# Kernel optimization log

Hardware: AMD Instinct MI355X
Metric: run time of the kernel (lower is better)

Reference implementation:

```python
import jax, jax.numpy as jnp
import numpy as np

N_NODES = 50000
N_EDGES = 400000
IN_DIM = 256
HID = 64
N_CLASSES = 121


def setup_inputs() -> dict:
    key = jax.random.key(0)
    ks = jax.random.split(key, 16)
    inp = {
        "features": jax.random.normal(ks[0], (N_NODES, IN_DIM), jnp.float32),
        "src": jax.random.randint(ks[1], (N_EDGES,), 0, N_NODES, jnp.int32),
        "dst": jax.random.randint(ks[2], (N_EDGES,), 0, N_NODES, jnp.int32),
        # layer 0: 4 heads, in_dim -> hid, no residual
        "W0": jax.random.normal(ks[3], (4, HID, IN_DIM), jnp.float32) * 0.05,
        "al0": jax.random.normal(ks[4], (4, HID), jnp.float32) * 0.05,
        "ar0": jax.random.normal(ks[5], (4, HID), jnp.float32) * 0.05,
        # layer 1: 4 heads, 4*hid -> hid, residual via fc
        "W1": jax.random.normal(ks[6], (4, HID, 4 * HID), jnp.float32) * 0.05,
        "al1": jax.random.normal(ks[7], (4, HID), jnp.float32) * 0.05,
        "ar1": jax.random.normal(ks[8], (4, HID), jnp.float32) * 0.05,
        "R1": jax.random.normal(ks[9], (4, HID, 4 * HID), jnp.float32) * 0.05,
        # final: 6 heads, 4*hid -> classes, residual via fc, averaged
        "Wf": jax.random.normal(ks[10], (6, N_CLASSES, 4 * HID), jnp.float32) * 0.05,
        "alf": jax.random.normal(ks[11], (6, N_CLASSES), jnp.float32) * 0.05,
        "arf": jax.random.normal(ks[12], (6, N_CLASSES), jnp.float32) * 0.05,
        "Rf": jax.random.normal(ks[13], (6, N_CLASSES, 4 * HID), jnp.float32) * 0.05,
    }
    return inp


def _gat_layer(x, src, dst, W, al, ar, R, n_nodes):
    """Multi-head GAT layer. x:[N,D], W:[H,K,D], al/ar:[H,K], R:[H,K,D] or None.
    Returns [N,H,K] = activation(residual + edge-softmax-weighted neighbor sum)."""
    ft = jnp.einsum('nd,hkd->nhk', x, W)              # [N,H,K]
    a1 = jnp.einsum('nhk,hk->nh', ft, al)             # [N,H] attn_l(ft)
    a2 = jnp.einsum('nhk,hk->nh', ft, ar)             # [N,H] attn_r(ft)
    # per-edge score: leaky_relu(a1[dst] + a2[src]) (DGL mailbox softmax over in-edges)
    s = jax.nn.leaky_relu(a1[dst] + a2[src], negative_slope=0.01)   # [E,H]
    smax = jax.ops.segment_max(s, dst, num_segments=n_nodes)        # [N,H]
    smax = jnp.where(jnp.isfinite(smax), smax, 0.0)
    ex = jnp.exp(s - smax[dst])                                     # [E,H]
    denom = jax.ops.segment_sum(ex, dst, num_segments=n_nodes)      # [N,H]
    msg = ex[:, :, None] * ft[src]                                  # [E,H,K]
    accum = jax.ops.segment_sum(msg, dst, num_segments=n_nodes)     # [N,H,K]
    accum = accum / jnp.where(denom > 0, denom, 1.0)[:, :, None]
    if R is not None:
        accum = accum + jnp.einsum('nd,hkd->nhk', x, R)
    return jax.nn.elu(accum)


def reference(features, src, dst, W0, al0, ar0, W1, al1, ar1, R1, Wf, alf, arf, Rf):
    n = features.shape[0]
    h0 = _gat_layer(features, src, dst, W0, al0, ar0, None, n)  # [N,4,64]
    h0 = h0.reshape(n, -1)                                      # concat heads -> [N,256]
    h1 = _gat_layer(h0, src, dst, W1, al1, ar1, R1, n)          # [N,4,64]
    h1 = h1.reshape(n, -1)                                      # [N,256]
    hf = _gat_layer(h1, src, dst, Wf, alf, arf, Rf, n)          # [N,6,121]
    return hf.mean(axis=1)                                      # average final heads -> [N,121]
```

## Files before the change

### kernel.cpp

```cpp
#include <hip/hip_runtime.h>
#include <math.h>

#define NN 50000
#define NE 400000
#define NB ((NN + 255) / 256)

typedef __attribute__((ext_vector_type(8))) short bf16x8;
typedef __attribute__((ext_vector_type(4))) float f32x4;
#define AS1 __attribute__((address_space(1)))
#define AS3 __attribute__((address_space(3)))

__device__ __forceinline__ float lrelu(float x){ return x > 0.0f ? x : 0.01f*x; }
__device__ __forceinline__ float eluf(float x){ return x > 0.0f ? x : __expf(x)-1.0f; }
__device__ __forceinline__ float bf2f(unsigned short u){
  union{unsigned i; float f;} v; v.i = ((unsigned)u)<<16; return v.f;
}
__device__ __forceinline__ unsigned short f2bf(float x){
  union{float f; unsigned i;} v; v.f = x;
  unsigned r = v.i + 0x7FFFu + ((v.i>>16)&1u);
  return (unsigned short)(r>>16);
}
__device__ __forceinline__ unsigned pack2(float a, float b){
  return (unsigned)f2bf(a) | ((unsigned)f2bf(b)<<16);
}
__device__ __forceinline__ float lo16(unsigned u){ return bf2f((unsigned short)(u & 0xffffu)); }
__device__ __forceinline__ float hi16(unsigned u){ return bf2f((unsigned short)(u >> 16)); }

__global__ void k_diag(float* out, float val){ out[0] = val; }

__global__ void k_cvt(const float* __restrict__ in, unsigned short* __restrict__ o, int n){
  int i = (blockIdx.x*256 + threadIdx.x)*4;
  if(i + 3 < n){
    float4 v = *(const float4*)(in + i);
    uint2 p; p.x = pack2(v.x, v.y); p.y = pack2(v.z, v.w);
    *(uint2*)(o + i) = p;
  } else {
    for(int k = i; k < n; k++) o[k] = f2bf(in[k]);
  }
}

__global__ void k_cvt3(const float* __restrict__ s0, const float* __restrict__ s1,
    const float* __restrict__ s2, unsigned short* __restrict__ d0,
    unsigned short* __restrict__ d1, unsigned short* __restrict__ d2, int n){
  const float* in = (blockIdx.y == 0) ? s0 : (blockIdx.y == 1) ? s1 : s2;
  unsigned short* o = (blockIdx.y == 0) ? d0 : (blockIdx.y == 1) ? d1 : d2;
  int i = (blockIdx.x*256 + threadIdx.x)*4;
  if(i + 3 < n){
    float4 v = *(const float4*)(in + i);
    uint2 p; p.x = pack2(v.x, v.y); p.y = pack2(v.z, v.w);
    *(uint2*)(o + i) = p;
  } else {
    for(int k = i; k < n; k++) o[k] = f2bf(in[k]);
  }
}

__global__ void k_cvt2(const float* __restrict__ s0, const float* __restrict__ s1,
    unsigned short* __restrict__ d0, unsigned short* __restrict__ d1, int n){
  const float* in = (blockIdx.y == 0) ? s0 : s1;
  unsigned short* o = (blockIdx.y == 0) ? d0 : d1;
  int i = (blockIdx.x*256 + threadIdx.x)*4;
  if(i + 3 < n){
    float4 v = *(const float4*)(in + i);
    uint2 p; p.x = pack2(v.x, v.y); p.y = pack2(v.z, v.w);
    *(uint2*)(o + i) = p;
  } else {
    for(int k = i; k < n; k++) o[k] = f2bf(in[k]);
  }
}

__global__ void k_foldAll(const float* __restrict__ W0, const float* __restrict__ al0, const float* __restrict__ ar0,
    const float* __restrict__ W1, const float* __restrict__ al1, const float* __restrict__ ar1,
    const float* __restrict__ Wf, const float* __restrict__ alf, const float* __restrict__ arf,
    float* __restrict__ fl0, float* __restrict__ fr0, float* __restrict__ fl1, float* __restrict__ fr1,
    float* __restrict__ flF, float* __restrict__ frF){
  int b = blockIdx.x, d = threadIdx.x;
  const float *W, *al, *ar; float *fl, *fr; int K, h;
  if(b < 4){ W=W0; al=al0; ar=ar0; fl=fl0; fr=fr0; K=64; h=b; }
  else if(b < 8){ W=W1; al=al1; ar=ar1; fl=fl1; fr=fr1; K=64; h=b-4; }
  else { W=Wf; al=alf; ar=arf; fl=flF; fr=frF; K=121; h=b-8; }
  float sl = 0.f, sr = 0.f;
  const float* wb = W + ((size_t)h*K)*256 + d;
  for(int k = 0; k < K; k++){
    float w = wb[(size_t)k*256];
    sl += al[h*K + k]*w;
    sr += ar[h*K + k]*w;
  }
  fl[h*256 + d] = sl;
  fr[h*256 + d] = sr;
}

__global__ void k_count(const int* __restrict__ dst, int* __restrict__ cnt, int E){
  int e = blockIdx.x * 256 + threadIdx.x;
  if(e < E) atomicAdd(&cnt[dst[e]], 1);
}

__global__ void k_scanA(const int* __restrict__ cnt, int* __restrict__ row_ptr,
    int* __restrict__ bsum, int N){
  __shared__ int sh[256];
  int t = threadIdx.x;
  int i = blockIdx.x*256 + t;
  int v = (i < N) ? cnt[i] : 0;
  sh[t] = v;
  __syncthreads();
  for(int off = 1; off < 256; off <<= 1){
    int u = (t >= off) ? sh[t - off] : 0;
    __syncthreads();
    sh[t] += u;
    __syncthreads();
  }
  if(i < N) row_ptr[i] = sh[t] - v;
  if(t == 255) bsum[blockIdx.x] = sh[255];
}

__global__ void k_scanB(const int* __restrict__ bsum, int* __restrict__ boff, int nb){
  __shared__ int sh[256];
  int t = threadIdx.x;
  int v = (t < nb) ? bsum[t] : 0;
  sh[t] = v;
  __syncthreads();
  for(int off = 1; off < 256; off <<= 1){
    int u = (t >= off) ? sh[t - off] : 0;
    __syncthreads();
    sh[t] += u;
    __syncthreads();
  }
  if(t < nb) boff[t] = sh[t] - v;
  if(t == 255) boff[nb] = sh[255];
}

__global__ void k_scanC(int* __restrict__ row_ptr, const int* __restrict__ boff, int N, int nb){
  int i = blockIdx.x*256 + threadIdx.x;
  if(i < N) row_ptr[i] += boff[blockIdx.x];
  if(i == 0) row_ptr[N] = boff[nb];
}

__global__ void k_scatter(const int* __restrict__ src, const int* __restrict__ dst,
    const int* __restrict__ row_ptr, int* __restrict__ cur,
    int* __restrict__ col_src, int* __restrict__ col_dst, int E){
  int e = blockIdx.x * 256 + threadIdx.x;
  if(e < E){
    int d = dst[e];
    int pos = row_ptr[d] + atomicAdd(&cur[d], 1);
    col_src[pos] = src[e];
    col_dst[pos] = d;
  }
}

template<int S>
__global__ __launch_bounds__(256) void k_eexp(const int* __restrict__ col_src, const int* __restrict__ col_dst,
    const float* __restrict__ a1, const float* __restrict__ a2, float* __restrict__ ex){
  int p = blockIdx.x*256 + threadIdx.x;
  if(p >= NE) return;
  int s = col_src[p], d = col_dst[p];
  if(S == 4){
    float4 v1 = *(const float4*)(a1 + (size_t)d*4);
    float4 v2 = *(const float4*)(a2 + (size_t)s*4);
    float4 o;
    o.x = __expf(lrelu(v1.x + v2.x));
    o.y = __expf(lrelu(v1.y + v2.y));
    o.z = __expf(lrelu(v1.z + v2.z));
    o.w = __expf(lrelu(v1.w + v2.w));
    *(float4*)(ex + (size_t)p*4) = o;
  } else {
    float4 l1 = *(const float4*)(a1 + (size_t)d*8);
    float2 h1 = *(const float2*)(a1 + (size_t)d*8 + 4);
    float4 l2 = *(const float4*)(a2 + (size_t)s*8);
    float2 h2 = *(const float2*)(a2 + (size_t)s*8 + 4);
    float4 o;
    o.x = __expf(lrelu(l1.x + l2.x));
    o.y = __expf(lrelu(l1.y + l2.y));
    o.z = __expf(lrelu(l1.z + l2.z));
    o.w = __expf(lrelu(l1.w + l2.w));
    float2 o2;
    o2.x = __expf(lrelu(h1.x + h2.x));
    o2.y = __expf(lrelu(h1.y + h2.y));
    *(float4*)(ex + (size_t)p*8) = o;
    *(float2*)(ex + (size_t)p*8 + 4) = o2;
  }
}

__global__ __launch_bounds__(256) void k_gemm16(const unsigned short* __restrict__ X,
    const unsigned short* __restrict__ W, unsigned short* __restrict__ out,
    int N, int Kout, int ostride){
  __shared__ unsigned short sA[4096];
  __shared__ unsigned short sB[4096];
  int tid = threadIdx.x;
  int l = tid & 63, w = tid >> 6;
  int wm = w >> 1, wn = w & 1;
  int row0 = blockIdx.x*128, col0 = blockIdx.y*128;

  f32x4 acc[4][4];
  #pragma unroll
  for(int i=0;i<4;i++)
    #pragma unroll
    for(int j=0;j<4;j++) acc[i][j] = (f32x4){0.f,0.f,0.f,0.f};

  int grA0 = row0 + l;        if(grA0 >= N) grA0 = 0;
  int grA1 = row0 + 64 + l;   if(grA1 >= N) grA1 = 0;
  int gcB0 = col0 + l;        if(gcB0 >= Kout) gcB0 = 0;
  int gcB1 = col0 + 64 + l;   if(gcB1 >= Kout) gcB1 = 0;
  const unsigned short* pa0 = X + (size_t)grA0*256 + w*8;
  const unsigned short* pa1 = X + (size_t)grA1*256 + w*8;
  const unsigned short* pb0 = W + (size_t)gcB0*256 + w*8;
  const unsigned short* pb1 = W + (size_t)gcB1*256 + w*8;

  AS3 unsigned short* a3A = (AS3 unsigned short*)sA;
  AS3 unsigned short* a3B = (AS3 unsigned short*)sB;

  for(int kt = 0; kt < 256; kt += 32){
    __builtin_amdgcn_global_load_lds((const AS1 void*)(pa0 + kt), (AS3 void*)(a3A + w*1024),       16, 0, 0);
    __builtin_amdgcn_global_load_lds((const AS1 void*)(pa1 + kt), (AS3 void*)(a3A + w*1024 + 512), 16, 0, 0);
    __builtin_amdgcn_global_load_lds((const AS1 void*)(pb0 + kt), (AS3 void*)(a3B + w*1024),       16, 0, 0);
    __builtin_amdgcn_global_load_lds((const AS1 void*)(pb1 + kt), (AS3 void*)(a3B + w*1024 + 512), 16, 0, 0);
    __syncthreads();
    bf16x8 af[4], bfr[4];
    #pragma unroll
    for(int f=0; f<4; f++){
      af[f]  = *(const bf16x8*)(sA + (l>>4)*1024 + (wm*64 + f*16 + (l&15))*8);
      bfr[f] = *(const bf16x8*)(sB + (l>>4)*1024 + (wn*64 + f*16 + (l&15))*8);
    }
    #pragma unroll
    for(int i=0;i<4;i++)
      #pragma unroll
      for(int j=0;j<4;j++)
        acc[i][j] = __builtin_amdgcn_mfma_f32_16x16x32_bf16(af[i], bfr[j], acc[i][j], 0, 0, 0);
    __syncthreads();
  }

  #pragma unroll
  for(int i=0;i<4;i++){
    int rbase = row0 + wm*64 + i*16 + (l>>4)*4;
    #pragma unroll
    for(int j=0;j<4;j++){
      int c = col0 + wn*64 + j*16 + (l&15);
      if(c < Kout){
        #pragma unroll
        for(int q=0;q<4;q++){
          int r = rbase + q;
          if(r < N) out[(size_t)r*ostride + c] = f2bf(acc[i][j][q]);
        }
      }
    }
  }
}

__global__ __launch_bounds__(256) void k_gemmFh(const unsigned short* __restrict__ aggX,
    const unsigned short* __restrict__ xin, const unsigned short* __restrict__ wf,
    const unsigned short* __restrict__ rf, float* __restrict__ outp, int M){
  __shared__ unsigned short sA[8192];
  __shared__ unsigned short sB[8192];
  int tid = threadIdx.x;
  int l = tid & 63, w = tid >> 6;
  int wm = w >> 1, wn = w & 1;
  int h = blockIdx.y;
  int row0 = blockIdx.x*128;
  int rA0 = row0 + l;      if(rA0 >= M) rA0 = 0;
  int rA1 = row0 + 64 + l; if(rA1 >= M) rA1 = 0;
  int cB1 = 64 + l; if(cB1 > 120) cB1 = 120;

  AS3 unsigned short* a3A = (AS3 unsigned short*)sA;
  AS3 unsigned short* a3B = (AS3 unsigned short*)sB;

  f32x4 acc[4][4];
  #pragma unroll
  for(int i=0;i<4;i++)
    #pragma unroll
    for(int j=0;j<4;j++) acc[i][j] = (f32x4){0.f,0.f,0.f,0.f};

  #pragma unroll 1
  for(int ph = 0; ph < 2; ph++){
    const unsigned short* pa0 = (ph ? xin + (size_t)rA0*256 : aggX + (size_t)rA0*1536 + h*256) + w*8;
    const unsigned short* pa1 = (ph ? xin + (size_t)rA1*256 : aggX + (size_t)rA1*1536 + h*256) + w*8;
    const unsigned short* pbb = (ph ? rf : wf) + (size_t)h*121*256;
    const unsigned short* pb0 = pbb + (size_t)l*256 + w*8;
    const unsigned short* pb1 = pbb + (size_t)cB1*256 + w*8;
    #pragma unroll 1
    for(int kt = 0; kt < 256; kt += 64){
      #pragma unroll
      for(int jj = 0; jj < 2; jj++){
        int j = w + jj*4;
        int ko = kt + jj*32;
        __builtin_amdgcn_global_load_lds((const AS1 void*)(pa0 + ko), (AS3 void*)(a3A + j*1024),       16, 0, 0);
        __builtin_amdgcn_global_load_lds((const AS1 void*)(pa1 + ko), (AS3 void*)(a3A + j*1024 + 512), 16, 0, 0);
        __builtin_amdgcn_global_load_lds((const AS1 void*)(pb0 + ko), (AS3 void*)(a3B + j*1024),       16, 0, 0);
        __builtin_amdgcn_global_load_lds((const AS1 void*)(pb1 + ko), (AS3 void*)(a3B + j*1024 + 512), 16, 0, 0);
      }
      __syncthreads();
      #pragma unroll
      for(int ks = 0; ks < 2; ks++){
        bf16x8 af[4], bfr[4];
        #pragma unroll
        for(int f=0; f<4; f++){
          af[f]  = *(const bf16x8*)(sA + (ks*4 + (l>>4))*1024 + (wm*64 + f*16 + (l&15))*8);
          bfr[f] = *(const bf16x8*)(sB + (ks*4 + (l>>4))*1024 + (wn*64 + f*16 + (l&15))*8);
        }
        #pragma unroll
        for(int i=0;i<4;i++)
          #pragma unroll
          for(int j=0;j<4;j++)
            acc[i][j] = __builtin_amdgcn_mfma_f32_16x16x32_bf16(af[i], bfr[j], acc[i][j], 0, 0, 0);
      }
      __syncthreads();
    }
  }

  const float inv6 = 1.0f/6.0f;
  #pragma unroll
  for(int i=0;i<4;i++){
    int rbase = row0 + wm*64 + i*16 + (l>>4)*4;
    #pragma unroll
    for(int j=0;j<4;j++){
      int c = wn*64 + j*16 + (l&15);
      if(c < 121){
        #pragma unroll
        for(int q=0;q<4;q++){
          int r = rbase + q;
          if(r < M) atomicAdd(&outp[(size_t)r*121 + c], eluf(acc[i][j][q]) * inv6);
        }
      }
    }
  }
}

template<int H, int OS>
__global__ __launch_bounds__(256) void k_a12dot(const unsigned short* __restrict__ x,
    const float* __restrict__ fl, const float* __restrict__ fr,
    float* __restrict__ a1, float* __restrict__ a2){
  int n = blockIdx.x*4 + (threadIdx.x>>6);
  if(n >= NN) return;
  int l = threadIdx.x & 63;
  uint2 rv = *(const uint2*)(x + (size_t)n*256 + l*4);
  float c0 = lo16(rv.x), c1 = hi16(rv.x), c2 = lo16(rv.y), c3 = hi16(rv.y);
  float s1[H], s2[H];
  #pragma unroll
  for(int h = 0; h < H; h++){
    float4 vl = *(const float4*)(fl + h*256 + l*4);
    float4 vr = *(const float4*)(fr + h*256 + l*4);
    s1[h] = c0*vl.x + c1*vl.y + c2*vl.z + c3*vl.w;
    s2[h] = c0*vr.x + c1*vr.y + c2*vr.z + c3*vr.w;
  }
  #pragma unroll
  for(int off = 32; off > 0; off >>= 1){
    #pragma unroll
    for(int h = 0; h < H; h++){
      s1[h] += __shfl_xor(s1[h], off);
      s2[h] += __shfl_xor(s2[h], off);
    }
  }
  if(l == 0){
    #pragma unroll
    for(int h = 0; h < H; h++){ a1[(size_t)n*OS + h] = s1[h]; a2[(size_t)n*OS + h] = s2[h]; }
  }
}

template<bool HAS_RES, int NH, int NOS>
__global__ __launch_bounds__(256) void k_agg4(const unsigned short* __restrict__ ft, int fts,
    const float* __restrict__ ex4,
    const int* __restrict__ row_ptr, const int* __restrict__ col_src,
    const unsigned short* __restrict__ res, int rs, unsigned short* __restrict__ outp,
    const float* __restrict__ nfl, const float* __restrict__ nfr,
    float* __restrict__ na1, float* __restrict__ na2){
  int n = blockIdx.x*4 + (threadIdx.x>>6);
  if(n >= NN) return;
  int l = threadIdx.x & 63;
  int h = l >> 4;
  int e0 = row_ptr[n], e1 = row_ptr[n+1];
  float acc0=0.f, acc1=0.f, acc2=0.f, acc3=0.f, d=0.f;
  int e = e0;
  for(; e + 4 <= e1; e += 4){
    int s0 = col_src[e], s1 = col_src[e+1], s2 = col_src[e+2], s3 = col_src[e+3];
    float x0 = ex4[(size_t)(e+0)*4 + h];
    float x1 = ex4[(size_t)(e+1)*4 + h];
    float x2 = ex4[(size_t)(e+2)*4 + h];
    float x3 = ex4[(size_t)(e+3)*4 + h];
    uint2 r0 = *(const uint2*)(ft + (size_t)s0*fts + l*4);
    uint2 r1 = *(const uint2*)(ft + (size_t)s1*fts + l*4);
    uint2 r2 = *(const uint2*)(ft + (size_t)s2*fts + l*4);
    uint2 r3 = *(const uint2*)(ft + (size_t)s3*fts + l*4);
    d += (x0 + x1) + (x2 + x3);
    acc0 += x0*lo16(r0.x) + x1*lo16(r1.x) + x2*lo16(r2.x) + x3*lo16(r3.x);
    acc1 += x0*hi16(r0.x) + x1*hi16(r1.x) + x2*hi16(r2.x) + x3*hi16(r3.x);
    acc2 += x0*lo16(r0.y) + x1*lo16(r1.y) + x2*lo16(r2.y) + x3*lo16(r3.y);
    acc3 += x0*hi16(r0.y) + x1*hi16(r1.y) + x2*hi16(r2.y) + x3*hi16(r3.y);
  }
  for(; e < e1; ++e){
    int s = col_src[e];
    float x = ex4[(size_t)e*4 + h];
    d += x;
    uint2 rv = *(const uint2*)(ft + (size_t)s*fts + l*4);
    acc0 += x*lo16(rv.x); acc1 += x*hi16(rv.x);
    acc2 += x*lo16(rv.y); acc3 += x*hi16(rv.y);
  }
  float inv = (e1 > e0) ? 1.0f/d : 0.0f;
  float v0 = acc0*inv, v1 = acc1*inv, v2 = acc2*inv, v3 = acc3*inv;
  if(HAS_RES){
    uint2 rr = *(const uint2*)(res + (size_t)n*rs + l*4);
    v0 += lo16(rr.x); v1 += hi16(rr.x); v2 += lo16(rr.y); v3 += hi16(rr.y);
  }
  float o0 = eluf(v0), o1 = eluf(v1), o2 = eluf(v2), o3 = eluf(v3);
  uint2 o;
  o.x = pack2(o0, o1);
  o.y = pack2(o2, o3);
  *(uint2*)(outp + (size_t)n*256 + l*4) = o;

  float s1[NH], s2[NH];
  #pragma unroll
  for(int hh = 0; hh < NH; hh++){
    float4 vl = *(const float4*)(nfl + hh*256 + l*4);
    float4 vr = *(const float4*)(nfr + hh*256 + l*4);
    s1[hh] = o0*vl.x + o1*vl.y + o2*vl.z + o3*vl.w;
    s2[hh] = o0*vr.x + o1*vr.y + o2*vr.z + o3*vr.w;
  }
  #pragma unroll
  for(int off = 32; off > 0; off >>= 1){
    #pragma unroll
    for(int hh = 0; hh < NH; hh++){
      s1[hh] += __shfl_xor(s1[hh], off);
      s2[hh] += __shfl_xor(s2[hh], off);
    }
  }
  if(l == 0){
    #pragma unroll
    for(int hh = 0; hh < NH; hh++){
      na1[(size_t)n*NOS + hh] = s1[hh];
      na2[(size_t)n*NOS + hh] = s2[hh];
    }
  }
}

__global__ __launch_bounds__(256) void k_aggx6(const unsigned short* __restrict__ x,
    const float* __restrict__ ex6,
    const int* __restrict__ row_ptr, const int* __restrict__ col_src,
    unsigned short* __restrict__ aggX){
  int n = blockIdx.x*4 + (threadIdx.x>>6);
  if(n >= NN) return;
  int l = threadIdx.x & 63;
  int e0 = row_ptr[n], e1 = row_ptr[n+1];
  float acc[6][4];
  float d[6];
  #pragma unroll
  for(int h=0;h<6;h++){ d[h]=0.f; acc[h][0]=0.f; acc[h][1]=0.f; acc[h][2]=0.f; acc[h][3]=0.f; }
  int e = e0;
  for(; e + 2 <= e1; e += 2){
    int s0 = col_src[e], s1 = col_src[e+1];
    float4 xl0 = *(const float4*)(ex6 + (size_t)(e+0)*8);
    float2 xh0 = *(const float2*)(ex6 + (size_t)(e+0)*8 + 4);
    float4 xl1 = *(const float4*)(ex6 + (size_t)(e+1)*8);
    float2 xh1 = *(const float2*)(ex6 + (size_t)(e+1)*8 + 4);
    uint2 rv0 = *(const uint2*)(x + (size_t)s0*256 + l*4);
    uint2 rv1 = *(const uint2*)(x + (size_t)s1*256 + l*4);
    float ex0[6] = {xl0.x, xl0.y, xl0.z, xl0.w, xh0.x, xh0.y};
    float ex1[6] = {xl1.x, xl1.y, xl1.z, xl1.w, xh1.x, xh1.y};
    float c00 = lo16(rv0.x), c01 = hi16(rv0.x), c02 = lo16(rv0.y), c03 = hi16(rv0.y);
    float c10 = lo16(rv1.x), c11 = hi16(rv1.x), c12 = lo16(rv1.y), c13 = hi16(rv1.y);
    #pragma unroll
    for(int h=0;h<6;h++){
      d[h] += ex0[h] + ex1[h];
      acc[h][0] += ex0[h]*c00 + ex1[h]*c10;
      acc[h][1] += ex0[h]*c01 + ex1[h]*c11;
      acc[h][2] += ex0[h]*c02 + ex1[h]*c12;
      acc[h][3] += ex0[h]*c03 + ex1[h]*c13;
    }
  }
  for(; e < e1; ++e){
    int s = col_src[e];
    float4 xl = *(const float4*)(ex6 + (size_t)e*8);
    float2 xh = *(const float2*)(ex6 + (size_t)e*8 + 4);
    uint2 rv = *(const uint2*)(x + (size_t)s*256 + l*4);
    float exv[6] = {xl.x, xl.y, xl.z, xl.w, xh.x, xh.y};
    float c0 = lo16(rv.x), c1 = hi16(rv.x), c2 = lo16(rv.y), c3 = hi16(rv.y);
    #pragma unroll
    for(int h=0;h<6;h++){
      d[h] += exv[h];
      acc[h][0] += exv[h]*c0;
      acc[h][1] += exv[h]*c1;
      acc[h][2] += exv[h]*c2;
      acc[h][3] += exv[h]*c3;
    }
  }
  bool deg = e1 > e0;
  #pragma unroll
  for(int h=0;h<6;h++){
    float inv = deg ? 1.0f/d[h] : 0.0f;
    uint2 o;
    o.x = pack2(acc[h][0]*inv, acc[h][1]*inv);
    o.y = pack2(acc[h][2]*inv, acc[h][3]*inv);
    *(uint2*)(aggX + (size_t)n*1536 + h*256 + l*4) = o;
  }
}

extern "C" void kernel_launch(void* const* d_in, const int* in_sizes, int n_in,
                              void* d_out, int out_size, void* d_ws, size_t ws_size,
                              hipStream_t stream){
  const float* features = (const float*)d_in[0];
  const int*   src      = (const int*)d_in[1];
  const int*   dst      = (const int*)d_in[2];
  const float* W0  = (const float*)d_in[3];
  const float* al0 = (const float*)d_in[4];
  const float* ar0 = (const float*)d_in[5];
  const float* W1  = (const float*)d_in[6];
  const float* al1 = (const float*)d_in[7];
  const float* ar1 = (const float*)d_in[8];
  const float* R1  = (const float*)d_in[9];
  const float* Wf  = (const float*)d_in[10];
  const float* alf = (const float*)d_in[11];
  const float* arf = (const float*)d_in[12];
  const float* Rf  = (const float*)d_in[13];
  float* out = (float*)d_out;
  (void)in_sizes; (void)n_in; (void)out_size;

  char* ws = (char*)d_ws;
  size_t off = 0;
  auto take = [&](size_t bytes) -> void* {
    void* p = ws + off;
    off += (bytes + 255) & ~(size_t)255;
    return p;
  };
  int* row_ptr = (int*)take((NN + 1) * sizeof(int));
  int* cur     = (int*)take(NN * sizeof(int));
  int* col_src = (int*)take(NE * sizeof(int));
  int* col_dst = (int*)take(NE * sizeof(int));
  int* bsum    = (int*)take(256 * sizeof(int));
  int* boff    = (int*)take(257 * sizeof(int));
  float* a1A = (float*)take((size_t)NN * 8 * sizeof(float));
  float* a2A = (float*)take((size_t)NN * 8 * sizeof(float));
  float* a1B = (float*)take((size_t)NN * 8 * sizeof(float));
  float* a2B = (float*)take((size_t)NN * 8 * sizeof(float));
  unsigned short* hB16   = (unsigned short*)take((size_t)NN * 256 * 2);
  unsigned short* ftres  = (unsigned short*)take((size_t)NN * 512 * 2);
  unsigned short* feat16 = (unsigned short*)take((size_t)NN * 256 * 2);
  unsigned short* hA16   = (unsigned short*)take((size_t)NN * 256 * 2);
  unsigned short* aggtl  = (unsigned short*)take((size_t)NN * 512 * 2);
  float* ex4 = (float*)take((size_t)NE * 4 * sizeof(float));
  float* ex6 = (float*)take((size_t)NE * 8 * sizeof(float));
  unsigned short* w016  = (unsigned short*)take(65536 * 2);
  unsigned short* w1r1  = (unsigned short*)take(131072 * 2);
  unsigned short* wf16  = (unsigned short*)take(185856 * 2);
  unsigned short* rf16  = (unsigned short*)take(185856 * 2);
  float* fl0 = (float*)take(4*256*sizeof(float));
  float* fr0 = (float*)take(4*256*sizeof(float));
  float* fl1 = (float*)take(4*256*sizeof(float));
  float* fr1 = (float*)take(4*256*sizeof(float));
  float* flF = (float*)take(6*256*sizeof(float));
  float* frF = (float*)take(6*256*sizeof(float));
  size_t need = off;
  (void)aggtl;

  if(ws_size < need){
    k_diag<<<1, 1, 0, stream>>>(out, 100.0f + (float)((double)ws_size / 1073741824.0));
    return;
  }

  unsigned short* aggX = ftres;

  hipMemsetAsync(cur, 0, NN * sizeof(int), stream);
  k_count<<<(NE + 255)/256, 256, 0, stream>>>(dst, cur, NE);
  k_scanA<<<NB, 256, 0, stream>>>(cur, row_ptr, bsum, NN);
  k_scanB<<<1, 256, 0, stream>>>(bsum, boff, NB);
  k_scanC<<<NB, 256, 0, stream>>>(row_ptr, boff, NN, NB);
  hipMemsetAsync(cur, 0, NN * sizeof(int), stream);
  k_scatter<<<(NE + 255)/256, 256, 0, stream>>>(src, dst, row_ptr, cur, col_src, col_dst, NE);

  k_cvt<<<(NN*256/4 + 255)/256, 256, 0, stream>>>(features, feat16, NN*256);
  k_cvt3<<<dim3(64, 3), 256, 0, stream>>>(W0, W1, R1, w016, w1r1, w1r1 + 65536, 65536);
  k_cvt2<<<dim3(182, 2), 256, 0, stream>>>(Wf, Rf, wf16, rf16, 185856);
  k_foldAll<<<14, 256, 0, stream>>>(W0, al0, ar0, W1, al1, ar1, Wf, alf, arf,
                                    fl0, fr0, fl1, fr1, flF, frF);

  int gm = (NN + 127) / 128;
  int gagg = (NN + 3) / 4;
  int gedge = (NE + 255) / 256;

  k_a12dot<4,4><<<gagg, 256, 0, stream>>>(feat16, fl0, fr0, a1A, a2A);
  k_eexp<4><<<gedge, 256, 0, stream>>>(col_src, col_dst, a1A, a2A, ex4);
  k_gemm16<<<dim3(gm, 2), 256, 0, stream>>>(feat16, w016, ftres, NN, 256, 256);
  k_agg4<false,4,4><<<gagg, 256, 0, stream>>>(ftres, 256, ex4, row_ptr, col_src,
      nullptr, 0, hA16, fl1, fr1, a1B, a2B);

  k_eexp<4><<<gedge, 256, 0, stream>>>(col_src, col_dst, a1B, a2B, ex4);
  k_gemm16<<<dim3(gm, 4), 256, 0, stream>>>(hA16, w1r1, ftres, NN, 512, 512);
  k_agg4<true,6,8><<<gagg, 256, 0, stream>>>(ftres, 512, ex4, row_ptr, col_src,
      ftres + 256, 512, hB16, flF, frF, a1A, a2A);

  k_eexp<8><<<gedge, 256, 0, stream>>>(col_src, col_dst, a1A, a2A, ex6);
  k_aggx6<<<gagg, 256, 0, stream>>>(hB16, ex6, row_ptr, col_src, aggX);
  hipMemsetAsync(out, 0, (size_t)NN * 121 * sizeof(float), stream);
  k_gemmFh<<<dim3(gm, 6), 256, 0, stream>>>(aggX, hB16, wf16, rf16, out, NN);
}
```

Measured before the change: 636.4 us.

## Chunk final GAT layer and replace output atomics with per-head partials plus reduce

The final layer's aggregation, GEMM and output stage now run in two chunks of 25000 nodes, so the intermediate aggregate buffer is half the size and more likely to stay cache-resident between the aggregation and GEMM kernels. Instead of six heads doing fp32 atomicAdd into the output, each head writes its ELU result as bf16 into a per-head partial buffer, and a new reduce kernel sums the six heads and scales by 1/6. This removes atomic contention and the output memset. In exchange it adds extra launches and partial-buffer traffic, and rounds head outputs to bf16 before summation, which costs some precision.

Result: faster. 514.6 us (-19.1%).

```diff
diff --git a/kernel.cpp b/kernel.cpp
--- a/kernel.cpp
+++ b/kernel.cpp
@@ -246,7 +246,7 @@
 
 __global__ __launch_bounds__(256) void k_gemmFh(const unsigned short* __restrict__ aggX,
     const unsigned short* __restrict__ xin, const unsigned short* __restrict__ wf,
-    const unsigned short* __restrict__ rf, float* __restrict__ outp, int M){
+    const unsigned short* __restrict__ rf, unsigned short* __restrict__ partial, int M){
   __shared__ unsigned short sA[8192];
   __shared__ unsigned short sB[8192];
   int tid = threadIdx.x;
@@ -304,22 +304,31 @@
     }
   }
 
-  const float inv6 = 1.0f/6.0f;
+  unsigned short* pb = partial + (size_t)h*M*128;
   #pragma unroll
   for(int i=0;i<4;i++){
     int rbase = row0 + wm*64 + i*16 + (l>>4)*4;
     #pragma unroll
     for(int j=0;j<4;j++){
       int c = wn*64 + j*16 + (l&15);
-      if(c < 121){
-        #pragma unroll
-        for(int q=0;q<4;q++){
-          int r = rbase + q;
-          if(r < M) atomicAdd(&outp[(size_t)r*121 + c], eluf(acc[i][j][q]) * inv6);
-        }
+      #pragma unroll
+      for(int q=0;q<4;q++){
+        int r = rbase + q;
+        if(r < M) pb[(size_t)r*128 + c] = f2bf(eluf(acc[i][j][q]));
       }
     }
   }
+}
+
+__global__ __launch_bounds__(256) void k_reduce6(const unsigned short* __restrict__ partial,
+    float* __restrict__ outp, int n0, int M){
+  int t = blockIdx.x*256 + threadIdx.x;
+  int idx = t >> 7, c = t & 127;
+  if(idx >= M || c >= 121) return;
+  float s = 0.f;
+  #pragma unroll
+  for(int h = 0; h < 6; h++) s += bf2f(partial[((size_t)h*M + idx)*128 + c]);
+  outp[(size_t)(n0 + idx)*121 + c] = s * (1.0f/6.0f);
 }
 
 template<int H, int OS>
@@ -431,9 +440,10 @@
 __global__ __launch_bounds__(256) void k_aggx6(const unsigned short* __restrict__ x,
     const float* __restrict__ ex6,
     const int* __restrict__ row_ptr, const int* __restrict__ col_src,
-    unsigned short* __restrict__ aggX){
-  int n = blockIdx.x*4 + (threadIdx.x>>6);
-  if(n >= NN) return;
+    unsigned short* __restrict__ aggX, int n0base, int M){
+  int idx = blockIdx.x*4 + (threadIdx.x>>6);
+  if(idx >= M) return;
+  int n = n0base + idx;
   int l = threadIdx.x & 63;
   int e0 = row_ptr[n], e1 = row_ptr[n+1];
   float acc[6][4];
@@ -485,7 +495,7 @@
     uint2 o;
     o.x = pack2(acc[h][0]*inv, acc[h][1]*inv);
     o.y = pack2(acc[h][2]*inv, acc[h][3]*inv);
-    *(uint2*)(aggX + (size_t)n*1536 + h*256 + l*4) = o;
+    *(uint2*)(aggX + (size_t)idx*1536 + h*256 + l*4) = o;
   }
 }
 
@@ -516,6 +526,7 @@
     off += (bytes + 255) & ~(size_t)255;
     return p;
   };
+  const int CH = 25000;
   int* row_ptr = (int*)take((NN + 1) * sizeof(int));
   int* cur     = (int*)take(NN * sizeof(int));
   int* col_src = (int*)take(NE * sizeof(int));
@@ -551,7 +562,8 @@
     return;
   }
 
-  unsigned short* aggX = ftres;
+  unsigned short* aggX    = ftres;
+  unsigned short* partial = hA16;
 
   hipMemsetAsync(cur, 0, NN * sizeof(int), stream);
   k_count<<<(NE + 255)/256, 256, 0, stream>>>(dst, cur, NE);
@@ -583,7 +595,10 @@
       ftres + 256, 512, hB16, flF, frF, a1A, a2A);
 
   k_eexp<8><<<gedge, 256, 0, stream>>>(col_src, col_dst, a1A, a2A, ex6);
-  k_aggx6<<<gagg, 256, 0, stream>>>(hB16, ex6, row_ptr, col_src, aggX);
-  hipMemsetAsync(out, 0, (size_t)NN * 121 * sizeof(float), stream);
-  k_gemmFh<<<dim3(gm, 6), 256, 0, stream>>>(aggX, hB16, wf16, rf16, out, NN);
-}
+  for(int c = 0; c < 2; c++){
+    int n0 = c*CH;
+    k_aggx6<<<(CH + 3)/4, 256, 0, stream>>>(hB16, ex6, row_ptr, col_src, aggX, n0, CH);
+    k_gemmFh<<<dim3((CH + 127)/128, 6), 256, 0, stream>>>(aggX, hB16 + (size_t)n0*256, wf16, rf16, partial, CH);
+    k_reduce6<<<(CH*128 + 255)/256, 256, 0, stream>>>(partial, out, n0, CH);
+  }
+}
```
